# Performance work log

Hardware: AMD Instinct MI355X
Metric: run time of the kernel (lower is better)

The kernel has to match this reference:

```python
import jax, jax.numpy as jnp
import numpy as np

# torch.optim.Adam defaults
LR = 1e-3
B1 = 0.9
B2 = 0.999
EPS = 1e-8


def setup_inputs() -> dict:
    key = jax.random.key(0)
    k1, k2 = jax.random.split(key)
    B, N_train, d = 128, 16384, 1024
    h = jax.random.normal(k1, (B, d), dtype=jnp.float32)
    H_train = jax.random.normal(k2, (N_train, d), dtype=jnp.float32)
    return {"h": h, "H_train": H_train, "n_epoch": 1000}


def reference(h, H_train, n_epoch):
    # preweights: [B, N_train], optimized by Adam for n_epoch steps
    B, N_train = h.shape[0], H_train.shape[0]

    def loss_fn(p):
        w = jax.nn.softmax(p, axis=-1)          # [B, N_train]
        H_approx = w @ H_train                   # [B, d]
        return jnp.sum((H_approx - h) ** 2)

    grad_fn = jax.grad(loss_fn)

    def step(carry, t):
        p, m, v = carry
        g = grad_fn(p)
        m = B1 * m + (1.0 - B1) * g
        v = B2 * v + (1.0 - B2) * (g * g)
        m_hat = m / (1.0 - B1 ** t)
        v_hat = v / (1.0 - B2 ** t)
        p = p - LR * m_hat / (jnp.sqrt(v_hat) + EPS)
        return (p, m, v), None

    z = jnp.zeros((B, N_train), dtype=jnp.float32)
    ts = jnp.arange(1, n_epoch + 1, dtype=jnp.float32)
    (p, _, _), _ = jax.lax.scan(step, (z, z, z), ts)
    return jax.nn.softmax(p, axis=-1)
```

## Files before the change

kernel.cpp:

```cpp
#include <hip/hip_runtime.h>
#include <math.h>

#define BB 128
#define NTR 16384
#define DD 1024
#define PN (BB*NTR)
#define CN (BB*DD)
#define HN (NTR*DD)
#define FWD_SLABS 64
#define BWD_SLABS 2

typedef short bf16x8 __attribute__((ext_vector_type(8)));
typedef float f32x2  __attribute__((ext_vector_type(2)));
typedef float f32x4v __attribute__((ext_vector_type(4)));

__device__ __forceinline__ ushort f2bf(float f) {
  uint u = __float_as_uint(f);
  return (ushort)((u + 0x7FFFu + ((u >> 16) & 1u)) >> 16);
}
__device__ __forceinline__ float bf2f(ushort h) { return __uint_as_float(((uint)h) << 16); }
__device__ __forceinline__ void split2(float f, ushort& a, ushort& b) {
  a = f2bf(f); float r1 = f - bf2f(a);
  b = f2bf(r1);
}

__global__ __launch_bounds__(256) void k_prep(const float* __restrict__ H,
    ushort* __restrict__ H0, ushort* __restrict__ H1)
{
  const size_t i = ((size_t)blockIdx.x * 256 + threadIdx.x) * 4;
  const float4 x = *(const float4*)(H + i);
  ushort a[4], b[4];
  split2(x.x, a[0], b[0]); split2(x.y, a[1], b[1]);
  split2(x.z, a[2], b[2]); split2(x.w, a[3], b[3]);
  *(ushort4*)(H0 + i) = make_ushort4(a[0], a[1], a[2], a[3]);
  *(ushort4*)(H1 + i) = make_ushort4(b[0], b[1], b[2], b[3]);
}

__global__ __launch_bounds__(256) void k_stat0(float* __restrict__ pmx, float* __restrict__ psm) {
  const int i = blockIdx.x * 256 + threadIdx.x;
  pmx[i] = 0.f;
  psm[i] = 2048.f;
}

__device__ __forceinline__ void combine_stats(const float* __restrict__ pmx,
    const float* __restrict__ psm, int row, float& mx, float& inv)
{
  mx = -INFINITY;
#pragma unroll
  for (int c = 0; c < 8; ++c) mx = fmaxf(mx, pmx[c*128 + row]);
  float s = 0.f;
#pragma unroll
  for (int c = 0; c < 8; ++c) s += psm[c*128 + row] * expf(pmx[c*128 + row] - mx);
  inv = 1.0f / s;
}

__global__ __launch_bounds__(512) void k_softmax_f(const float* __restrict__ p,
                                                   float* __restrict__ w) {
  const int row = blockIdx.x, tid = threadIdx.x;
  const float* pr = p + (size_t)row * NTR;
  float x[32]; float mx = -INFINITY;
#pragma unroll
  for (int i = 0; i < 32; ++i) { x[i] = pr[i*512 + tid]; mx = fmaxf(mx, x[i]); }
  __shared__ float red[512];
  red[tid] = mx; __syncthreads();
  for (int s = 256; s > 0; s >>= 1) { if (tid < s) red[tid] = fmaxf(red[tid], red[tid+s]); __syncthreads(); }
  mx = red[0]; __syncthreads();
  float sum = 0.f;
#pragma unroll
  for (int i = 0; i < 32; ++i) { x[i] = expf(x[i] - mx); sum += x[i]; }
  red[tid] = sum; __syncthreads();
  for (int s = 256; s > 0; s >>= 1) { if (tid < s) red[tid] += red[tid+s]; __syncthreads(); }
  const float inv = 1.0f / red[0];
  float* wr = w + (size_t)row * NTR;
#pragma unroll
  for (int i = 0; i < 32; ++i) wr[i*512 + tid] = x[i] * inv;
}

__global__ __launch_bounds__(256) void k_fwd_v(const float* __restrict__ p,
    const float* __restrict__ pmx, const float* __restrict__ psm,
    const float* __restrict__ H, float* __restrict__ Cp)
{
  const int nt = blockIdx.x, tid = threadIdx.x;
  const int kbase = blockIdx.y * 256;
  Cp += (size_t)blockIdx.y * CN;
  __shared__ float As[8][128];
  __shared__ float Bs[8][128];
  __shared__ float smx[128], sinv[128];
  if (tid < 128) {
    float mx, inv; combine_stats(pmx, psm, tid, mx, inv);
    smx[tid] = mx; sinv[tid] = inv;
  }
  const int tm = tid >> 4, tn = tid & 15;
  const int m0 = tm * 8, n0 = tn * 8;
  const int mm = tid >> 1, q = tid & 1;
  const int br = tid >> 5, bc = (tid & 31) * 4;
  const float* Asrc = p + (size_t)mm*NTR + kbase + q*4;
  const float* Bsrc = H + (size_t)(kbase+br)*DD + nt*128 + bc;
  __syncthreads();
  const float mxv = smx[mm], invv = sinv[mm];

  f32x2 acc[8][4];
#pragma unroll
  for (int i = 0; i < 8; ++i)
#pragma unroll
    for (int j = 0; j < 4; ++j) acc[i][j] = (f32x2){0.f, 0.f};

  float4 ra = *(const float4*)(Asrc);
  float4 rb = *(const float4*)(Bsrc);
  float4 wa = make_float4(expf(ra.x-mxv)*invv, expf(ra.y-mxv)*invv,
                          expf(ra.z-mxv)*invv, expf(ra.w-mxv)*invv);
  for (int kk = 0; kk < 256; kk += 8) {
    __syncthreads();
    As[q*4+0][mm]=wa.x; As[q*4+1][mm]=wa.y; As[q*4+2][mm]=wa.z; As[q*4+3][mm]=wa.w;
    *(float4*)&Bs[br][bc] = rb;
    __syncthreads();
    if (kk + 8 < 256) {
      ra = *(const float4*)(Asrc + kk + 8);
      rb = *(const float4*)(Bsrc + (size_t)(kk+8)*DD);
      wa = make_float4(expf(ra.x-mxv)*invv, expf(ra.y-mxv)*invv,
                       expf(ra.z-mxv)*invv, expf(ra.w-mxv)*invv);
    }
#pragma unroll
    for (int k = 0; k < 8; ++k) {
      float a[8];
      *(float4*)&a[0] = *(const float4*)&As[k][m0];
      *(float4*)&a[4] = *(const float4*)&As[k][m0+4];
      f32x2 b[4];
      b[0] = *(const f32x2*)&Bs[k][n0];
      b[1] = *(const f32x2*)&Bs[k][n0+2];
      b[2] = *(const f32x2*)&Bs[k][n0+4];
      b[3] = *(const f32x2*)&Bs[k][n0+6];
#pragma unroll
      for (int i = 0; i < 8; ++i) {
        const f32x2 ai = (f32x2){a[i], a[i]};
#pragma unroll
        for (int j = 0; j < 4; ++j)
          acc[i][j] = __builtin_elementwise_fma(ai, b[j], acc[i][j]);
      }
    }
  }
#pragma unroll
  for (int i = 0; i < 8; ++i) {
    float* dst = Cp + (size_t)(m0+i)*DD + nt*128 + n0;
    *(float4*)dst     = make_float4(acc[i][0].x, acc[i][0].y, acc[i][1].x, acc[i][1].y);
    *(float4*)(dst+4) = make_float4(acc[i][2].x, acc[i][2].y, acc[i][3].x, acc[i][3].y);
  }
}

__global__ __launch_bounds__(256) void k_reduce_S2s(const float* __restrict__ X,
    const float* __restrict__ h,
    ushort* __restrict__ s0, ushort* __restrict__ s1)
{
  const size_t off = ((size_t)blockIdx.x * 256 + threadIdx.x) * 2;
  f32x2 s = (f32x2){0.f, 0.f};
#pragma unroll 4
  for (int k = 0; k < FWD_SLABS; ++k) {
    const f32x2 c = *(const f32x2*)(X + (size_t)k * CN + off);
    s.x += c.x; s.y += c.y;
  }
  const f32x2 hh = *(const f32x2*)(h + off);
  float v0 = 2.f*(s.x-hh.x), v1 = 2.f*(s.y-hh.y);
  ushort a0, b0, a1, b1;
  split2(v0, a0, b0); split2(v1, a1, b1);
  *(ushort2*)(s0 + off) = make_ushort2(a0, a1);
  *(ushort2*)(s1 + off) = make_ushort2(b0, b1);
}

__global__ __launch_bounds__(256, 2) void k_gemm3_bwd(
    const ushort* __restrict__ A0, const ushort* __restrict__ A1,
    const ushort* __restrict__ B0, const ushort* __restrict__ B1,
    const float* __restrict__ p,
    const float* __restrict__ pmx, const float* __restrict__ psm,
    float* __restrict__ C, float* __restrict__ rpart)
{
  __shared__ ushort lds[12288];
  __shared__ float rbuf[128][33];
  __shared__ float smx[128], sinv[128];
  const int tid = threadIdx.x;
  const int lane = tid & 63, wid = tid >> 6;
  const int wm = (wid >> 1) * 64, wn = (wid & 1) * 32;
  const int bn = blockIdx.x, ks = blockIdx.y;
  const int n0 = bn * 64;
  const int kbase = ks * 512;
  C += (size_t)ks * PN;

  const ushort* Ap[2] = {A0, A1};
  const ushort* Bp[2] = {B0, B1};

  f32x4v acc[4][2];
#pragma unroll
  for (int i = 0; i < 4; ++i)
#pragma unroll
    for (int j = 0; j < 2; ++j) acc[i][j] = (f32x4v){0.f, 0.f, 0.f, 0.f};

  for (int kt = 0; kt < 16; ++kt) {
    const int kpos = kbase + (kt << 5);
#pragma unroll
    for (int c = 0; c < 4; ++c) {
      const int L = c*256 + tid;
      const int s = L >> 9, rr = L & 511;
      const int row = rr >> 2, slot = rr & 3;
      const int sl = slot ^ ((row >> 1) & 3);
      const ushort* src = Ap[s] + (size_t)row * DD + kpos + (sl << 3);
      __builtin_amdgcn_global_load_lds((const __attribute__((address_space(1))) void*)src,
          (__attribute__((address_space(3))) void*)&lds[(size_t)(c*256 + (wid << 6)) * 8], 16, 0, 0);
    }
#pragma unroll
    for (int c = 0; c < 2; ++c) {
      const int L = c*256 + tid;
      const int s = L >> 8, rr = L & 255;
      const int row = rr >> 2, slot = rr & 3;
      const int sl = slot ^ ((row >> 1) & 3);
      const ushort* src = Bp[s] + (size_t)(n0 + row) * DD + kpos + (sl << 3);
      __builtin_amdgcn_global_load_lds((const __attribute__((address_space(1))) void*)src,
          (__attribute__((address_space(3))) void*)&lds[8192 + (size_t)(c*256 + (wid << 6)) * 8], 16, 0, 0);
    }
    __syncthreads();

    bf16x8 bf[2][2];
#pragma unroll
    for (int s = 0; s < 2; ++s)
#pragma unroll
      for (int j = 0; j < 2; ++j) {
        const int n = wn + j*16 + (lane & 15);
        const int sl = (lane >> 4) ^ ((n >> 1) & 3);
        bf[s][j] = *(const bf16x8*)&lds[8192 + s*2048 + n*32 + sl*8];
      }
#pragma unroll
    for (int sa = 0; sa < 2; ++sa) {
      bf16x8 af[4];
#pragma unroll
      for (int i = 0; i < 4; ++i) {
        const int mrow = wm + i*16 + (lane & 15);
        const int sl = (lane >> 4) ^ ((mrow >> 1) & 3);
        af[i] = *(const bf16x8*)&lds[sa*4096 + mrow*32 + sl*8];
      }
#pragma unroll
      for (int sb = 0; sb < 2 - sa; ++sb)
#pragma unroll
        for (int i = 0; i < 4; ++i)
#pragma unroll
          for (int j = 0; j < 2; ++j)
            acc[i][j] = __builtin_amdgcn_mfma_f32_16x16x32_bf16(af[i], bf[sb][j], acc[i][j], 0, 0, 0);
    }
    __syncthreads();
  }
  if (tid < 128) {
    float mx, inv; combine_stats(pmx, psm, tid, mx, inv);
    smx[tid] = mx; sinv[tid] = inv;
  }
  __syncthreads();
#pragma unroll
  for (int i = 0; i < 4; ++i) {
    const int rbase = wm + i*16 + ((lane >> 4) << 2);
#pragma unroll
    for (int r = 0; r < 4; ++r) {
      const int row = rbase + r;
      const float mxv = smx[row], invv = sinv[row];
      float s = 0.f;
#pragma unroll
      for (int j = 0; j < 2; ++j) {
        const int cg = n0 + wn + j*16 + (lane & 15);
        C[(size_t)row * NTR + cg] = acc[i][j][r];
        const float wv = expf(p[(size_t)row * NTR + cg] - mxv) * invv;
        s = fmaf(wv, acc[i][j][r], s);
      }
      rbuf[row][((wn >> 5) << 4) + (lane & 15)] = s;
    }
  }
  __syncthreads();
  if (tid < 128) {
    float s = 0.f;
#pragma unroll
    for (int t = 0; t < 32; ++t) s += rbuf[tid][t];
    rpart[(size_t)tid * 512 + ks*256 + bn] = s;
  }
}

__global__ __launch_bounds__(256) void k_adam_f(float* __restrict__ pp_,
    float* __restrict__ m, float* __restrict__ v,
    const float* __restrict__ X, const float* __restrict__ rpart,
    const float* __restrict__ pmx_in, const float* __restrict__ psm_in,
    float* __restrict__ pmx_out, float* __restrict__ psm_out,
    float bc1, float bc2)
{
  const int bid = blockIdx.x, tid = threadIdx.x;
  const int row = bid >> 3, chunk = bid & 7;
  float mx, inv; combine_stats(pmx_in, psm_in, row, mx, inv);
  __shared__ float red[256];
  red[tid] = rpart[(size_t)row*512 + tid] + rpart[(size_t)row*512 + 256 + tid];
  __syncthreads();
  for (int s = 128; s > 0; s >>= 1) { if (tid < s) red[tid] += red[tid+s]; __syncthreads(); }
  const float rr = red[0];
  const size_t base = (size_t)bid * 2048 + tid * 4;
  float pn[8];
#pragma unroll
  for (int part = 0; part < 2; ++part) {
    const size_t off = base + part * 1024;
    float4 u  = *(const float4*)(X + off);
    const float4 u1 = *(const float4*)(X + (size_t)PN + off);
    u.x += u1.x; u.y += u1.y; u.z += u1.z; u.w += u1.w;
    const float uu[4] = {u.x, u.y, u.z, u.w};
    float4 p4 = *(float4*)(pp_ + off);
    float4 m4 = *(float4*)(m + off);
    float4 v4 = *(float4*)(v + off);
    float* pp = (float*)&p4; float* mm = (float*)&m4; float* vv = (float*)&v4;
#pragma unroll
    for (int e = 0; e < 4; ++e) {
      const float wv = expf(pp[e] - mx) * inv;
      const float g  = wv * (uu[e] - rr);
      const float mn = 0.9f*mm[e] + 0.1f*g;
      const float vn = 0.999f*vv[e] + 0.001f*(g*g);
      const float mh = mn / bc1, vh = vn / bc2;
      pp[e] = pp[e] - 1e-3f * mh / (sqrtf(vh) + 1e-8f);
      mm[e] = mn; vv[e] = vn;
      pn[part*4 + e] = pp[e];
    }
    *(float4*)(pp_ + off) = p4;
    *(float4*)(m + off) = m4;
    *(float4*)(v + off) = v4;
  }
  float lmx = pn[0];
#pragma unroll
  for (int e = 1; e < 8; ++e) lmx = fmaxf(lmx, pn[e]);
  __syncthreads();
  red[tid] = lmx; __syncthreads();
  for (int s = 128; s > 0; s >>= 1) { if (tid < s) red[tid] = fmaxf(red[tid], red[tid+s]); __syncthreads(); }
  const float bmx = red[0]; __syncthreads();
  float ls = 0.f;
#pragma unroll
  for (int e = 0; e < 8; ++e) ls += expf(pn[e] - bmx);
  red[tid] = ls; __syncthreads();
  for (int s = 128; s > 0; s >>= 1) { if (tid < s) red[tid] += red[tid+s]; __syncthreads(); }
  if (tid == 0) {
    pmx_out[chunk*128 + row] = bmx;
    psm_out[chunk*128 + row] = red[0];
  }
}

extern "C" void kernel_launch(void* const* d_in, const int* in_sizes, int n_in,
                              void* d_out, int out_size, void* d_ws, size_t ws_size,
                              hipStream_t stream) {
  const float* h = (const float*)d_in[0];
  const float* H = (const float*)d_in[1];
  (void)in_sizes; (void)n_in; (void)out_size; (void)ws_size;
  const int n_epoch = 1000;

  float* p  = (float*)d_ws;
  float* m  = p + PN;
  float* v  = m + PN;
  float* X  = v + PN;
  float* rp = X + (size_t)4*PN;
  float* pmxA = rp + 128*512;
  float* psmA = pmxA + 1024;
  float* pmxB = psmA + 1024;
  float* psmB = pmxB + 1024;
  ushort* s0 = (ushort*)(psmB + 1024);
  ushort* s1 = s0 + CN;
  ushort* H0 = s1 + CN, *H1 = H0 + HN;

  hipMemsetAsync(p, 0, (size_t)3*PN*sizeof(float), stream);
  k_prep<<<HN/1024, 256, 0, stream>>>(H, H0, H1);
  k_stat0<<<4, 256, 0, stream>>>(pmxA, psmA);

  for (int s = 1; s <= n_epoch; ++s) {
    float* pmx_in  = (s & 1) ? pmxA : pmxB;
    float* psm_in  = (s & 1) ? psmA : psmB;
    float* pmx_out = (s & 1) ? pmxB : pmxA;
    float* psm_out = (s & 1) ? psmB : psmA;
    k_fwd_v<<<dim3(8, FWD_SLABS), 256, 0, stream>>>(p, pmx_in, psm_in, H, X);
    k_reduce_S2s<<<CN/512, 256, 0, stream>>>(X, h, s0, s1);
    k_gemm3_bwd<<<dim3(256, BWD_SLABS), 256, 0, stream>>>(s0, s1, H0, H1, p, pmx_in, psm_in, X, rp);
    const float bc1 = 1.0f - powf(0.9f,   (float)s);
    const float bc2 = 1.0f - powf(0.999f, (float)s);
    k_adam_f<<<1024, 256, 0, stream>>>(p, m, v, X, rp, pmx_in, psm_in, pmx_out, psm_out, bc1, bc2);
  }
  k_softmax_f<<<BB, 512, 0, stream>>>(p, (float*)d_out);
}
```

Measured before the change: 112.5 ms.

## Materialize softmax weights once per step and double-buffer forward GEMM LDS

Adds a kernel that computes the softmax weight matrix once per step from the running max/sum stats, and passes it to the forward GEMM, backward epilogue and Adam kernels. Those kernels no longer each recompute expf. The forward GEMM also switches to a double-buffered LDS pipeline with one barrier per k-step. The cost is an extra full-size write and read of the weight matrix, plus one more launch per step.

```diff
diff --git a/kernel.cpp b/kernel.cpp
--- a/kernel.cpp
+++ b/kernel.cpp
@@ -54,6 +54,22 @@
   inv = 1.0f / s;
 }
 
+__global__ __launch_bounds__(256) void k_wmat(const float* __restrict__ p,
+    const float* __restrict__ pmx, const float* __restrict__ psm,
+    float* __restrict__ w)
+{
+  const int bid = blockIdx.x, tid = threadIdx.x;
+  const int row = bid >> 3;
+  float mx, inv; combine_stats(pmx, psm, row, mx, inv);
+  const size_t base = (size_t)bid * 2048 + tid * 8;
+  const float4 a = *(const float4*)(p + base);
+  const float4 b = *(const float4*)(p + base + 4);
+  *(float4*)(w + base)     = make_float4(expf(a.x-mx)*inv, expf(a.y-mx)*inv,
+                                         expf(a.z-mx)*inv, expf(a.w-mx)*inv);
+  *(float4*)(w + base + 4) = make_float4(expf(b.x-mx)*inv, expf(b.y-mx)*inv,
+                                         expf(b.z-mx)*inv, expf(b.w-mx)*inv);
+}
+
 __global__ __launch_bounds__(512) void k_softmax_f(const float* __restrict__ p,
                                                    float* __restrict__ w) {
   const int row = blockIdx.x, tid = threadIdx.x;
@@ -76,28 +92,20 @@
   for (int i = 0; i < 32; ++i) wr[i*512 + tid] = x[i] * inv;
 }
 
-__global__ __launch_bounds__(256) void k_fwd_v(const float* __restrict__ p,
-    const float* __restrict__ pmx, const float* __restrict__ psm,
+__global__ __launch_bounds__(256) void k_fwd_v(const float* __restrict__ w,
     const float* __restrict__ H, float* __restrict__ Cp)
 {
   const int nt = blockIdx.x, tid = threadIdx.x;
   const int kbase = blockIdx.y * 256;
   Cp += (size_t)blockIdx.y * CN;
-  __shared__ float As[8][128];
-  __shared__ float Bs[8][128];
-  __shared__ float smx[128], sinv[128];
-  if (tid < 128) {
-    float mx, inv; combine_stats(pmx, psm, tid, mx, inv);
-    smx[tid] = mx; sinv[tid] = inv;
-  }
+  __shared__ float As[2][8][128];
+  __shared__ float Bs[2][8][128];
   const int tm = tid >> 4, tn = tid & 15;
   const int m0 = tm * 8, n0 = tn * 8;
   const int mm = tid >> 1, q = tid & 1;
   const int br = tid >> 5, bc = (tid & 31) * 4;
-  const float* Asrc = p + (size_t)mm*NTR + kbase + q*4;
+  const float* Asrc = w + (size_t)mm*NTR + kbase + q*4;
   const float* Bsrc = H + (size_t)(kbase+br)*DD + nt*128 + bc;
-  __syncthreads();
-  const float mxv = smx[mm], invv = sinv[mm];
 
   f32x2 acc[8][4];
 #pragma unroll
@@ -107,29 +115,33 @@
 
   float4 ra = *(const float4*)(Asrc);
   float4 rb = *(const float4*)(Bsrc);
-  float4 wa = make_float4(expf(ra.x-mxv)*invv, expf(ra.y-mxv)*invv,
-                          expf(ra.z-mxv)*invv, expf(ra.w-mxv)*invv);
-  for (int kk = 0; kk < 256; kk += 8) {
+  As[0][q*4+0][mm]=ra.x; As[0][q*4+1][mm]=ra.y; As[0][q*4+2][mm]=ra.z; As[0][q*4+3][mm]=ra.w;
+  *(float4*)&Bs[0][br][bc] = rb;
+  ra = *(const float4*)(Asrc + 8);
+  rb = *(const float4*)(Bsrc + (size_t)8*DD);
+
+  for (int t = 0; t < 32; ++t) {
+    const int cur = t & 1;
     __syncthreads();
-    As[q*4+0][mm]=wa.x; As[q*4+1][mm]=wa.y; As[q*4+2][mm]=wa.z; As[q*4+3][mm]=wa.w;
-    *(float4*)&Bs[br][bc] = rb;
-    __syncthreads();
-    if (kk + 8 < 256) {
-      ra = *(const float4*)(Asrc + kk + 8);
-      rb = *(const float4*)(Bsrc + (size_t)(kk+8)*DD);
-      wa = make_float4(expf(ra.x-mxv)*invv, expf(ra.y-mxv)*invv,
-                       expf(ra.z-mxv)*invv, expf(ra.w-mxv)*invv);
+    if (t + 1 < 32) {
+      As[cur^1][q*4+0][mm]=ra.x; As[cur^1][q*4+1][mm]=ra.y;
+      As[cur^1][q*4+2][mm]=ra.z; As[cur^1][q*4+3][mm]=ra.w;
+      *(float4*)&Bs[cur^1][br][bc] = rb;
+    }
+    if (t + 2 < 32) {
+      ra = *(const float4*)(Asrc + (t+2)*8);
+      rb = *(const float4*)(Bsrc + (size_t)((t+2)*8)*DD);
     }
 #pragma unroll
     for (int k = 0; k < 8; ++k) {
       float a[8];
-      *(float4*)&a[0] = *(const float4*)&As[k][m0];
-      *(float4*)&a[4] = *(const float4*)&As[k][m0+4];
+      *(float4*)&a[0] = *(const float4*)&As[cur][k][m0];
+      *(float4*)&a[4] = *(const float4*)&As[cur][k][m0+4];
       f32x2 b[4];
-      b[0] = *(const f32x2*)&Bs[k][n0];
-      b[1] = *(const f32x2*)&Bs[k][n0+2];
-      b[2] = *(const f32x2*)&Bs[k][n0+4];
-      b[3] = *(const f32x2*)&Bs[k][n0+6];
+      b[0] = *(const f32x2*)&Bs[cur][k][n0];
+      b[1] = *(const f32x2*)&Bs[cur][k][n0+2];
+      b[2] = *(const f32x2*)&Bs[cur][k][n0+4];
+      b[3] = *(const f32x2*)&Bs[cur][k][n0+6];
 #pragma unroll
       for (int i = 0; i < 8; ++i) {
         const f32x2 ai = (f32x2){a[i], a[i]};
@@ -169,13 +181,11 @@
 __global__ __launch_bounds__(256, 2) void k_gemm3_bwd(
     const ushort* __restrict__ A0, const ushort* __restrict__ A1,
     const ushort* __restrict__ B0, const ushort* __restrict__ B1,
-    const float* __restrict__ p,
-    const float* __restrict__ pmx, const float* __restrict__ psm,
+    const float* __restrict__ w,
     float* __restrict__ C, float* __restrict__ rpart)
 {
   __shared__ ushort lds[12288];
   __shared__ float rbuf[128][33];
-  __shared__ float smx[128], sinv[128];
   const int tid = threadIdx.x;
   const int lane = tid & 63, wid = tid >> 6;
   const int wm = (wid >> 1) * 64, wn = (wid & 1) * 32;
@@ -245,25 +255,18 @@
     }
     __syncthreads();
   }
-  if (tid < 128) {
-    float mx, inv; combine_stats(pmx, psm, tid, mx, inv);
-    smx[tid] = mx; sinv[tid] = inv;
-  }
-  __syncthreads();
 #pragma unroll
   for (int i = 0; i < 4; ++i) {
     const int rbase = wm + i*16 + ((lane >> 4) << 2);
 #pragma unroll
     for (int r = 0; r < 4; ++r) {
       const int row = rbase + r;
-      const float mxv = smx[row], invv = sinv[row];
       float s = 0.f;
 #pragma unroll
       for (int j = 0; j < 2; ++j) {
         const int cg = n0 + wn + j*16 + (lane & 15);
         C[(size_t)row * NTR + cg] = acc[i][j][r];
-        const float wv = expf(p[(size_t)row * NTR + cg] - mxv) * invv;
-        s = fmaf(wv, acc[i][j][r], s);
+        s = fmaf(w[(size_t)row * NTR + cg], acc[i][j][r], s);
       }
       rbuf[row][((wn >> 5) << 4) + (lane & 15)] = s;
     }
@@ -279,14 +282,13 @@
 
 __global__ __launch_bounds__(256) void k_adam_f(float* __restrict__ pp_,
     float* __restrict__ m, float* __restrict__ v,
-    const float* __restrict__ X, const float* __restrict__ rpart,
-    const float* __restrict__ pmx_in, const float* __restrict__ psm_in,
+    const float* __restrict__ w, const float* __restrict__ X,
+    const float* __restrict__ rpart,
     float* __restrict__ pmx_out, float* __restrict__ psm_out,
     float bc1, float bc2)
 {
   const int bid = blockIdx.x, tid = threadIdx.x;
   const int row = bid >> 3, chunk = bid & 7;
-  float mx, inv; combine_stats(pmx_in, psm_in, row, mx, inv);
   __shared__ float red[256];
   red[tid] = rpart[(size_t)row*512 + tid] + rpart[(size_t)row*512 + 256 + tid];
   __syncthreads();
@@ -300,6 +302,8 @@
     float4 u  = *(const float4*)(X + off);
     const float4 u1 = *(const float4*)(X + (size_t)PN + off);
     u.x += u1.x; u.y += u1.y; u.z += u1.z; u.w += u1.w;
+    const float4 w4 = *(const float4*)(w + off);
+    const float wv[4] = {w4.x, w4.y, w4.z, w4.w};
     const float uu[4] = {u.x, u.y, u.z, u.w};
     float4 p4 = *(float4*)(pp_ + off);
     float4 m4 = *(float4*)(m + off);
@@ -307,8 +311,7 @@
     float* pp = (float*)&p4; float* mm = (float*)&m4; float* vv = (float*)&v4;
 #pragma unroll
     for (int e = 0; e < 4; ++e) {
-      const float wv = expf(pp[e] - mx) * inv;
-      const float g  = wv * (uu[e] - rr);
+      const float g  = wv[e] * (uu[e] - rr);
       const float mn = 0.9f*mm[e] + 0.1f*g;
       const float vn = 0.999f*vv[e] + 0.001f*(g*g);
       const float mh = mn / bc1, vh = vn / bc2;
@@ -349,7 +352,8 @@
   float* p  = (float*)d_ws;
   float* m  = p + PN;
   float* v  = m + PN;
-  float* X  = v + PN;
+  float* w  = v + PN;
+  float* X  = w + PN;
   float* rp = X + (size_t)4*PN;
   float* pmxA = rp + 128*512;
   float* psmA = pmxA + 1024;
@@ -368,12 +372,13 @@
     float* psm_in  = (s & 1) ? psmA : psmB;
     float* pmx_out = (s & 1) ? pmxB : pmxA;
     float* psm_out = (s & 1) ? psmB : psmA;
-    k_fwd_v<<<dim3(8, FWD_SLABS), 256, 0, stream>>>(p, pmx_in, psm_in, H, X);
+    k_wmat<<<PN/2048, 256, 0, stream>>>(p, pmx_in, psm_in, w);
+    k_fwd_v<<<dim3(8, FWD_SLABS), 256, 0, stream>>>(w, H, X);
     k_reduce_S2s<<<CN/512, 256, 0, stream>>>(X, h, s0, s1);
-    k_gemm3_bwd<<<dim3(256, BWD_SLABS), 256, 0, stream>>>(s0, s1, H0, H1, p, pmx_in, psm_in, X, rp);
+    k_gemm3_bwd<<<dim3(256, BWD_SLABS), 256, 0, stream>>>(s0, s1, H0, H1, w, X, rp);
     const float bc1 = 1.0f - powf(0.9f,   (float)s);
     const float bc2 = 1.0f - powf(0.999f, (float)s);
-    k_adam_f<<<1024, 256, 0, stream>>>(p, m, v, X, rp, pmx_in, psm_in, pmx_out, psm_out, bc1, bc2);
+    k_adam_f<<<1024, 256, 0, stream>>>(p, m, v, w, X, rp, pmx_out, psm_out, bc1, bc2);
   }
   k_softmax_f<<<BB, 512, 0, stream>>>(p, (float*)d_out);
 }
```

New measurement: 110.5 ms. No clear change (-1.8%).
